# Performance work log

Hardware: AMD Instinct MI355X
Metric: run time of the kernel (lower is better)

The kernel has to match this reference:

```python
import jax, jax.numpy as jnp
import numpy as np

C = 256
G = 32  # GroupNorm groups
EPS = 1e-6


def setup_inputs() -> dict:
    key = jax.random.key(0)
    ks = jax.random.split(key, 11)
    B, H, W = 4, 64, 64
    scale = 0.02
    return {
        "x": jax.random.normal(ks[0], (B, C, H, W), dtype=jnp.float32),
        "gn_scale": jnp.ones((C,), jnp.float32),
        "gn_bias": jnp.zeros((C,), jnp.float32),
        "wq": jax.random.normal(ks[1], (C, C), jnp.float32) * scale,
        "bq": jnp.zeros((C,), jnp.float32),
        "wk": jax.random.normal(ks[2], (C, C), jnp.float32) * scale,
        "bk": jnp.zeros((C,), jnp.float32),
        "wv": jax.random.normal(ks[3], (C, C), jnp.float32) * scale,
        "bv": jnp.zeros((C,), jnp.float32),
        "wp": jax.random.normal(ks[4], (C, C), jnp.float32) * scale,
        "bp": jnp.zeros((C,), jnp.float32),
    }


def _group_norm(x, scale, bias):
    b, c, h, w = x.shape
    xr = x.reshape(b, G, c // G, h, w)
    mu = jnp.mean(xr, axis=(2, 3, 4), keepdims=True)
    var = jnp.var(xr, axis=(2, 3, 4), keepdims=True)
    xn = ((xr - mu) * jax.lax.rsqrt(var + EPS)).reshape(b, c, h, w)
    return xn * scale[None, :, None, None] + bias[None, :, None, None]


def _conv1x1(x, w, bch):
    # 1x1 conv == channel-mixing matmul; w is (out_ch, in_ch)
    return jnp.einsum('bchw,dc->bdhw', x, w) + bch[None, :, None, None]


def reference(x, gn_scale, gn_bias, wq, bq, wk, bk, wv, bv, wp, bp):
    b, c, h, w = x.shape
    hn = _group_norm(x, gn_scale, gn_bias)
    q = _conv1x1(hn, wq, bq).reshape(b, c, h * w)  # (b,c,N)
    k = _conv1x1(hn, wk, bk).reshape(b, c, h * w)
    v = _conv1x1(hn, wv, bv).reshape(b, c, h * w)
    # attn[b,i,j] = softmax_j( q_i . k_j / sqrt(c) )
    attn = jax.nn.softmax(jnp.einsum('bci,bcj->bij', q, k) * (c ** -0.5), axis=-1)
    A = jnp.einsum('bcj,bij->bci', v, attn).reshape(b, c, h, w)
    return x + _conv1x1(A, wp, bp)
```

## Files before the change

### kernel.cpp

```cpp
#include <hip/hip_runtime.h>
#include <stdint.h>

#define Bn 4
#define Cn 256
#define Gn 32
#define Nn 4096
#define CGn 8

typedef unsigned short u16;
typedef __attribute__((ext_vector_type(8))) short short8;
typedef __attribute__((ext_vector_type(4))) short short4v;
typedef __attribute__((ext_vector_type(4))) float f32x4;
typedef __attribute__((ext_vector_type(16))) float f32x16;

__device__ __forceinline__ u16 f2bf(float x) {
  uint32_t u = __float_as_uint(x);
  u += 0x7fffu + ((u >> 16) & 1u);
  return (u16)(u >> 16);
}
__device__ __forceinline__ float b2f(u16 v) {
  return __uint_as_float(((uint32_t)v) << 16);
}

__device__ __forceinline__ void gl_lds16(const void* g, void* l) {
  __builtin_amdgcn_global_load_lds(
      (__attribute__((address_space(1))) void*)(uintptr_t)g,
      (__attribute__((address_space(3))) void*)(uintptr_t)l, 16, 0, 0);
}

__device__ __forceinline__ int sw512(int row, int cb) { return row * 512 + ((cb ^ (row & 7)) * 16); }

__global__ void k_cs(const float* __restrict__ wq, const float* __restrict__ wk,
                     const float* __restrict__ wv, const float* __restrict__ wp,
                     const float* __restrict__ bq, const float* __restrict__ bk,
                     const float* __restrict__ bv, const float* __restrict__ x,
                     u16* __restrict__ wqkv, u16* __restrict__ wpb,
                     float* __restrict__ bqkv, float* __restrict__ stats) {
  if (blockIdx.x < 256) {
    const float s = 0.09016844005556021f;
    int i = blockIdx.x * 256 + threadIdx.x;
    wqkv[i]          = f2bf(wq[i] * s);
    wqkv[i + 65536]  = f2bf(wk[i]);
    wqkv[i + 131072] = f2bf(wv[i]);
    wpb[i]           = f2bf(wp[i]);
    if (i < 256) { bqkv[i] = bq[i] * s; bqkv[i + 256] = bk[i]; bqkv[i + 512] = bv[i]; }
  } else {
    int blk = blockIdx.x - 256;
    int grp = blk >> 2, part = blk & 3;
    const float4* base = (const float4*)(x + (size_t)grp * (CGn * Nn) + part * 8192);
    float s = 0.f, s2 = 0.f;
    for (int i = threadIdx.x; i < 2048; i += 256) {
      float4 v = base[i];
      s  += v.x + v.y + v.z + v.w;
      s2 += v.x * v.x + v.y * v.y + v.z * v.z + v.w * v.w;
    }
#pragma unroll
    for (int m = 1; m < 64; m <<= 1) { s += __shfl_xor(s, m, 64); s2 += __shfl_xor(s2, m, 64); }
    __shared__ float ps[4], ps2[4];
    int w = threadIdx.x >> 6;
    if ((threadIdx.x & 63) == 0) { ps[w] = s; ps2[w] = s2; }
    __syncthreads();
    if (threadIdx.x == 0) {
      stats[grp * 8 + part * 2]     = ps[0] + ps[1] + ps[2] + ps[3];
      stats[grp * 8 + part * 2 + 1] = ps2[0] + ps2[1] + ps2[2] + ps2[3];
    }
  }
}

__global__ void k_apply(const float* __restrict__ x, const float* __restrict__ stats,
                        const float* __restrict__ gsc, const float* __restrict__ gbi,
                        u16* __restrict__ hnT) {
  __shared__ __align__(16) char smem[32768];
  __shared__ float smu[Gn], srs[Gn];
  int n0 = blockIdx.x * 64;
  int b = blockIdx.y;
  int tid = threadIdx.x;
  if (tid < Gn) {
    float S = 0.f, S2 = 0.f;
#pragma unroll
    for (int p = 0; p < 4; ++p) {
      S  += stats[(b * Gn + tid) * 8 + p * 2];
      S2 += stats[(b * Gn + tid) * 8 + p * 2 + 1];
    }
    const float inv = 1.f / (CGn * Nn);
    float mu = S * inv;
    float var = S2 * inv - mu * mu;
    smu[tid] = mu;
    srs[tid] = rsqrtf(var + 1e-6f);
  }
  __syncthreads();
  int nl = (tid & 15) * 4;
  int cbase = tid >> 4;
  for (int pass = 0; pass < 16; ++pass) {
    int c = pass * 16 + cbase;
    float4 v = *(const float4*)(x + (size_t)b * Cn * Nn + (size_t)c * Nn + n0 + nl);
    int g = c >> 3;
    float sc = gsc[c] * srs[g];
    float bi = gbi[c] - smu[g] * sc;
    float vals[4] = {v.x, v.y, v.z, v.w};
#pragma unroll
    for (int i = 0; i < 4; ++i) {
      int row = nl + i;
      int off = row * 512 + ((((c >> 3) + row) & 31) * 16) + (c & 7) * 2;
      *(u16*)(smem + off) = f2bf(vals[i] * sc + bi);
    }
  }
  __syncthreads();
#pragma unroll
  for (int p = 0; p < 8; ++p) {
    int idx = p * 256 + tid;
    int row = idx >> 5, pc = idx & 31;
    int gc = (pc - row) & 31;
    short8 v8 = *(const short8*)(smem + row * 512 + pc * 16);
    *(short8*)(hnT + ((size_t)b * Nn + n0 + row) * Cn + gc * 8) = v8;
  }
}

__global__ __launch_bounds__(256, 2)
void k_qkv(const u16* __restrict__ wqkv, const float* __restrict__ bqkv,
           const u16* __restrict__ hnT, u16* __restrict__ qT, u16* __restrict__ kT,
           u16* __restrict__ vv) {
  __shared__ __align__(16) char smem[65536];
  const int tid = threadIdx.x, lane = tid & 63, w = tid >> 6;
  const int quad = (lane >> 4) & 3, low = lane & 15;
  const int d0 = blockIdx.y * 64, b = blockIdx.z;
  const int n_base = blockIdx.x * 256;
  const int which = d0 >> 8;
  const int dl0 = d0 & 255;
  const u16* hb = hnT + (size_t)b * Nn * Cn;
  const int scol = lane & 31;

#define QKV_STAGE(bsel, nt)                                                     \
  {                                                                             \
    _Pragma("unroll") for (int s = 0; s < 8; ++s) {                             \
      int r = w * 16 + s * 2 + (lane >> 5);                                     \
      int gc = (scol - r) & 31;                                                 \
      gl_lds16(hb + (size_t)(n_base + (nt) * 64 + r) * Cn + gc * 8,             \
               smem + (bsel) * 32768 + (w * 16 + s * 2) * 512);                 \
    }                                                                           \
  }

  QKV_STAGE(0, 0);
  short8 af[8];
  {
    const u16* wrow = wqkv + (size_t)(d0 + w * 16 + low) * Cn + quad * 8;
#pragma unroll
    for (int kk = 0; kk < 8; ++kk) af[kk] = *(const short8*)(wrow + kk * 32);
  }
  float bias[4];
#pragma unroll
  for (int r = 0; r < 4; ++r) bias[r] = bqkv[d0 + w * 16 + quad * 4 + r];

  for (int nt = 0; nt < 4; ++nt) {
    if (nt < 3) {
      QKV_STAGE((nt + 1) & 1, nt + 1);
      asm volatile("s_waitcnt vmcnt(10)" ::: "memory");
    } else {
      asm volatile("s_waitcnt vmcnt(0)" ::: "memory");
    }
    asm volatile("s_barrier" ::: "memory");
    char* buf = smem + (nt & 1) * 32768;
    f32x4 acc[4] = {{0.f,0.f,0.f,0.f},{0.f,0.f,0.f,0.f},{0.f,0.f,0.f,0.f},{0.f,0.f,0.f,0.f}};
#pragma unroll
    for (int kk = 0; kk < 8; ++kk)
#pragma unroll
      for (int t = 0; t < 4; ++t) {
        int row = t * 16 + low;
        short8 bf = *(const short8*)(buf + row * 512 + (((kk * 4 + quad) + row) & 31) * 16);
        acc[t] = __builtin_amdgcn_mfma_f32_16x16x32_bf16(af[kk], bf, acc[t], 0, 0, 0);
      }
    asm volatile("s_barrier" ::: "memory");
    char* Q = buf + w * 8192;
    if (which == 2) {
#pragma unroll
      for (int t = 0; t < 4; ++t)
#pragma unroll
        for (int rp = 0; rp < 2; ++rp) {
          uint32_t wv2;
          float f0 = acc[t][2 * rp] + bias[2 * rp];
          float f1 = acc[t][2 * rp + 1] + bias[2 * rp + 1];
          asm("v_cvt_pk_bf16_f32 %0, %1, %2" : "=v"(wv2) : "v"(f0), "v"(f1));
          *(u16*)(Q + (quad * 4 + 2 * rp) * 144 + t * 32 + low * 2) = (u16)wv2;
          *(u16*)(Q + (quad * 4 + 2 * rp + 1) * 144 + t * 32 + low * 2) = (u16)(wv2 >> 16);
        }
#pragma unroll
      for (int s = 0; s < 2; ++s) {
        int slot = s * 64 + lane;
        int row = slot >> 3, ch = slot & 7;
        short8 v8 = *(const short8*)(Q + row * 144 + ch * 16);
        *(short8*)(vv + (size_t)b * Cn * Nn + (size_t)(dl0 + w * 16 + row) * Nn +
                   n_base + nt * 64 + ch * 8) = v8;
      }
    } else {
#pragma unroll
      for (int t = 0; t < 4; ++t) {
        union { uint32_t u[2]; short4v s; } pk;
        float f0 = acc[t][0] + bias[0], f1 = acc[t][1] + bias[1];
        float f2 = acc[t][2] + bias[2], f3 = acc[t][3] + bias[3];
        asm("v_cvt_pk_bf16_f32 %0, %1, %2" : "=v"(pk.u[0]) : "v"(f0), "v"(f1));
        asm("v_cvt_pk_bf16_f32 %0, %1, %2" : "=v"(pk.u[1]) : "v"(f2), "v"(f3));
        *(short4v*)(Q + (t * 16 + low) * 48 + quad * 8) = pk.s;
      }
      u16* dst = (which == 0 ? qT : kT) + (size_t)b * Nn * Cn;
#pragma unroll
      for (int s = 0; s < 2; ++s) {
        int slot = s * 64 + lane;
        int row = slot >> 1, half = slot & 1;
        short8 v8 = *(const short8*)(Q + row * 48 + half * 16);
        *(short8*)(dst + (size_t)(n_base + nt * 64 + row) * Cn + dl0 + w * 16 + half * 8) = v8;
      }
    }
  }
#undef QKV_STAGE
}

__device__ __forceinline__ void flash_stage(char* smem, int bsel, const u16* kTb,
                                            const u16* vb, int j0, int w, int lo,
                                            int kr, int vr, int vp) {
  char* ksb = smem + bsel * 32768;
  char* vsb = ksb + 16384;
#pragma unroll
  for (int s = 0; s < 4; ++s) {
    int j = kr + s * 2;
    int gc = (lo - j) & 31;
    gl_lds16(kTb + (size_t)(j0 + j) * Cn + gc * 8, ksb + (w * 8 + s * 2) * 512);
  }
#pragma unroll
  for (int s = 0; s < 4; ++s) {
    int c = vr + s * 16;
    int gc = (vp - c - (c >> 2)) & 3;
    gl_lds16(vb + (size_t)c * Nn + j0 + gc * 8, vsb + (w * 64 + s * 16) * 64);
  }
}

__global__ __launch_bounds__(256, 2)
void k_flash(const u16* __restrict__ qT, const u16* __restrict__ kT,
             const u16* __restrict__ vv, u16* __restrict__ Op0,
             u16* __restrict__ Op1, u16* __restrict__ Op2, u16* __restrict__ Op3,
             float* __restrict__ lrow) {
  __shared__ __align__(16) char smem[65536];
  const int tid = threadIdx.x, lane = tid & 63, w = tid >> 6;
  const int lo = lane & 31, hi = lane >> 5;
  const int i0 = blockIdx.x * 128;
  const int b = blockIdx.y, jh = blockIdx.z;
  const u16* qTb = qT + (size_t)b * Nn * Cn;
  const u16* kTb = kT + (size_t)b * Nn * Cn;
  const u16* vb  = vv + (size_t)b * Cn * Nn;
  const int u7 = lo + hi;
  const int u9 = lo + hi + (lo >> 2);
  const int kr = w * 8 + hi;
  const int vr = w * 64 + (lane >> 2);
  const int vp = lane & 3;

  flash_stage(smem, 0, kTb, vb, jh * 1024, w, lo, kr, vr, vp);

  short8 qf[16];
  {
    const u16* qrow = qTb + (size_t)(i0 + w * 32 + lo) * Cn + hi * 8;
#pragma unroll
    for (int ks = 0; ks < 16; ++ks) qf[ks] = *(const short8*)(qrow + ks * 16);
  }
  f32x16 Oa[8];
#pragma unroll
  for (int ct = 0; ct < 8; ++ct)
#pragma unroll
    for (int e = 0; e < 16; ++e) Oa[ct][e] = 0.f;
  float l_ = 0.f;

  for (int jt = 0; jt < 32; ++jt) {
    if (jt < 31) {
      flash_stage(smem, (jt + 1) & 1, kTb, vb, jh * 1024 + (jt + 1) * 32, w, lo, kr, vr, vp);
      asm volatile("s_waitcnt vmcnt(8)" ::: "memory");
    } else {
      asm volatile("s_waitcnt vmcnt(0)" ::: "memory");
    }
    asm volatile("s_barrier" ::: "memory");
    const char* ksb = smem + (jt & 1) * 32768;
    const char* vsb = ksb + 16384;

    f32x16 S0;
#pragma unroll
    for (int e = 0; e < 16; ++e) S0[e] = 0.f;
    __builtin_amdgcn_s_setprio(1);
#pragma unroll
    for (int ks = 0; ks < 16; ++ks) {
      int ch = (ks * 2 + u7) & 31;
      short8 a0 = *(const short8*)(ksb + lo * 512 + ch * 16);
      S0 = __builtin_amdgcn_mfma_f32_32x32x16_bf16(a0, qf[ks], S0, 0, 0, 0);
    }
    __builtin_amdgcn_s_setprio(0);
    uint32_t Pp[8];
#pragma unroll
    for (int g = 0; g < 8; ++g) {
      float p0 = __builtin_amdgcn_exp2f(S0[2 * g]);
      float p1 = __builtin_amdgcn_exp2f(S0[2 * g + 1]);
      l_ += p0 + p1;
      asm("v_cvt_pk_bf16_f32 %0, %1, %2" : "=v"(Pp[g]) : "v"(p0), "v"(p1));
    }
#pragma unroll
    for (int kst = 0; kst < 2; ++kst) {
      uint32_t x0 = Pp[4 * kst], x1 = Pp[4 * kst + 1];
      uint32_t y0 = Pp[4 * kst + 2], y1 = Pp[4 * kst + 3];
      asm("v_permlane32_swap_b32 %0, %1" : "+v"(x0), "+v"(y0));
      asm("v_permlane32_swap_b32 %0, %1" : "+v"(x1), "+v"(y1));
      union { uint32_t u[4]; short8 s8; } pu;
      pu.u[0] = x0;
      pu.u[1] = x1;
      pu.u[2] = y0;
      pu.u[3] = y1;
      int ch = (kst * 2 + u9) & 3;
      __builtin_amdgcn_s_setprio(1);
#pragma unroll
      for (int ct = 0; ct < 8; ++ct) {
        short8 vf = *(const short8*)(vsb + (ct * 32 + lo) * 64 + ch * 16);
        Oa[ct] = __builtin_amdgcn_mfma_f32_32x32x16_bf16(vf, pu.s8, Oa[ct], 0, 0, 0);
      }
      __builtin_amdgcn_s_setprio(0);
    }
    asm volatile("s_barrier" ::: "memory");
  }

  l_ += __shfl_xor(l_, 32, 64);
  if (hi == 0)
    lrow[(size_t)jh * (Bn * Nn) + (size_t)b * Nn + i0 + w * 32 + lo] = l_;
  float invl = __builtin_amdgcn_rcpf(l_);
  __syncthreads();
#pragma unroll
  for (int ct = 0; ct < 8; ++ct)
#pragma unroll
    for (int g = 0; g < 4; ++g) {
      union { uint32_t u[2]; short4v s; } pk;
      float f0 = Oa[ct][g * 4 + 0] * invl, f1 = Oa[ct][g * 4 + 1] * invl;
      float f2 = Oa[ct][g * 4 + 2] * invl, f3 = Oa[ct][g * 4 + 3] * invl;
      asm("v_cvt_pk_bf16_f32 %0, %1, %2" : "=v"(pk.u[0]) : "v"(f0), "v"(f1));
      asm("v_cvt_pk_bf16_f32 %0, %1, %2" : "=v"(pk.u[1]) : "v"(f2), "v"(f3));
      int chv = (ct * 4 + g + lo) & 31;
      *(short4v*)(smem + w * 16384 + lo * 512 + chv * 16 + hi * 8) = pk.s;
    }
  __syncthreads();
  u16* Opj = (jh == 0) ? Op0 : (jh == 1) ? Op1 : (jh == 2) ? Op2 : Op3;
  u16* Ob = Opj + ((size_t)b * Nn + i0 + w * 32) * (size_t)Cn;
#pragma unroll
  for (int s = 0; s < 16; ++s) {
    int rr = s * 2 + hi;
    short8 v8 = *(const short8*)(smem + w * 16384 + rr * 512 + lo * 16);
    int gc = (lo - rr) & 31;
    *(short8*)(Ob + (size_t)rr * Cn + gc * 8) = v8;
  }
}

__global__ __launch_bounds__(256, 2)
void k_proj(const u16* __restrict__ wpb, const float* __restrict__ bp,
            const u16* __restrict__ O0, const u16* __restrict__ O1,
            const u16* __restrict__ O2, const u16* __restrict__ O3,
            const float* __restrict__ lrow,
            const float* __restrict__ x, float* __restrict__ out) {
  __shared__ __align__(16) char smem[65536];
  int tid = threadIdx.x, lane = tid & 63, w = tid >> 6, quad = lane >> 4, low = lane & 15;
  int n0 = blockIdx.x * 64, d0 = blockIdx.y * 64, b = blockIdx.z;
  {
    int r0 = w * 16;
#pragma unroll
    for (int s = 0; s < 8; ++s) {
      int rs = r0 + s * 2;
      int r = rs + (lane >> 5);
      int cb = (lane & 31) ^ (r & 7);
      gl_lds16(wpb + (size_t)(d0 + r) * Cn + cb * 8, smem + rs * 512);
    }
  }
#pragma unroll 4
  for (int p = 0; p < 8; ++p) {
    int slot = p * 256 + tid;
    int row = slot >> 5, pc = slot & 31;
    int gcb = pc ^ (row & 7);
    size_t gbase = ((size_t)b * Nn + n0 + row) * Cn + gcb * 8;
    short8 a0 = *(const short8*)(O0 + gbase);
    short8 a1 = *(const short8*)(O1 + gbase);
    short8 a2 = *(const short8*)(O2 + gbase);
    short8 a3 = *(const short8*)(O3 + gbase);
    int rrow = b * Nn + n0 + row;
    float L = lrow[rrow] + lrow[Bn * Nn + rrow] + lrow[2 * Bn * Nn + rrow] +
              lrow[3 * Bn * Nn + rrow];
    float inv = __builtin_amdgcn_rcpf(L);
    short8 o;
#pragma unroll
    for (int i = 0; i < 8; ++i)
      o[i] = (short)f2bf((b2f((u16)a0[i]) + b2f((u16)a1[i]) + b2f((u16)a2[i]) +
                          b2f((u16)a3[i])) * inv);
    *(short8*)(smem + 32768 + row * 512 + pc * 16) = o;
  }
  asm volatile("s_waitcnt vmcnt(0)" ::: "memory");
  __syncthreads();
  f32x4 acc[4] = {{0.f,0.f,0.f,0.f},{0.f,0.f,0.f,0.f},{0.f,0.f,0.f,0.f},{0.f,0.f,0.f,0.f}};
#pragma unroll
  for (int kk = 0; kk < 8; ++kk) {
    short8 af = *(const short8*)(smem + sw512(w * 16 + low, kk * 4 + quad));
#pragma unroll
    for (int t = 0; t < 4; ++t) {
      short8 bf = *(const short8*)(smem + 32768 + sw512(t * 16 + low, kk * 4 + quad));
      acc[t] = __builtin_amdgcn_mfma_f32_16x16x32_bf16(af, bf, acc[t], 0, 0, 0);
    }
  }
  int dloc = d0 + w * 16 + quad * 4;
#pragma unroll
  for (int t = 0; t < 4; ++t)
#pragma unroll
    for (int r = 0; r < 4; ++r) {
      size_t idx = (size_t)b * Cn * Nn + (size_t)(dloc + r) * Nn + n0 + t * 16 + low;
      out[idx] = x[idx] + acc[t][r] + bp[dloc + r];
    }
}

extern "C" void kernel_launch(void* const* d_in, const int* in_sizes, int n_in,
                              void* d_out, int out_size, void* d_ws, size_t ws_size,
                              hipStream_t stream) {
  const float* x   = (const float*)d_in[0];
  const float* gsc = (const float*)d_in[1];
  const float* gbi = (const float*)d_in[2];
  const float* wq  = (const float*)d_in[3];
  const float* bq  = (const float*)d_in[4];
  const float* wk  = (const float*)d_in[5];
  const float* bk  = (const float*)d_in[6];
  const float* wv  = (const float*)d_in[7];
  const float* bv  = (const float*)d_in[8];
  const float* wp  = (const float*)d_in[9];
  const float* bp  = (const float*)d_in[10];
  float* out = (float*)d_out;

  char* ws = (char*)d_ws;
  u16*   wqkv  = (u16*)(ws + 0);
  u16*   wpb   = (u16*)(ws + 393216);
  float* bqkv  = (float*)(ws + 524288);
  float* stats = (float*)(ws + 527360);
  float* lrow  = (float*)(ws + 532480);
  u16*   hnT   = (u16*)(ws + 1048576);
  u16*   qT    = (u16*)(ws + 9437184);
  u16*   kT    = (u16*)(ws + 17825792);
  u16*   vv    = (u16*)(ws + 26214400);
  u16*   Op1   = (u16*)(ws + 34603008);
  u16*   Op2   = (u16*)(ws + 42991616);
  u16*   Op3   = (u16*)(ws + 51380224);

  k_cs<<<768, 256, 0, stream>>>(wq, wk, wv, wp, bq, bk, bv, x, wqkv, wpb, bqkv, stats);
  k_apply<<<dim3(64, 4), 256, 0, stream>>>(x, stats, gsc, gbi, hnT);
  k_qkv<<<dim3(16, 12, 4), 256, 0, stream>>>(wqkv, bqkv, hnT, qT, kT, vv);
  k_flash<<<dim3(32, 4, 4), 256, 0, stream>>>(qT, kT, vv, hnT , Op1, Op2, Op3, lrow);
  k_proj<<<dim3(64, 4, 4), 256, 0, stream>>>(wpb, bp, hnT , Op1, Op2, Op3, lrow, x, out);
}
```

Baseline: 191.2 us.

## Fuse GroupNorm apply into QKV projection kernel, dropping hnT intermediate

Removes the separate k_apply kernel. k_qkv now reads fp32 x directly, normalizes it with the group stats, converts it to bf16 into LDS, and runs the MFMA projection on that tile, so the bf16 hnT buffer is never written or read back. The async double-buffered LDS staging is replaced by synchronous loads with barriers, shared memory shrinks, and launch bounds rise to 3 blocks per SM. The trade-off is redundant work: each of the 12 d-blocks re-reads and re-normalizes the same x tile, raising global fp32 traffic and losing load/compute overlap.

```diff
diff --git a/kernel.cpp b/kernel.cpp
--- a/kernel.cpp
+++ b/kernel.cpp
@@ -67,80 +67,35 @@
   }
 }
 
-__global__ void k_apply(const float* __restrict__ x, const float* __restrict__ stats,
-                        const float* __restrict__ gsc, const float* __restrict__ gbi,
-                        u16* __restrict__ hnT) {
-  __shared__ __align__(16) char smem[32768];
-  __shared__ float smu[Gn], srs[Gn];
-  int n0 = blockIdx.x * 64;
-  int b = blockIdx.y;
-  int tid = threadIdx.x;
-  if (tid < Gn) {
-    float S = 0.f, S2 = 0.f;
-#pragma unroll
-    for (int p = 0; p < 4; ++p) {
-      S  += stats[(b * Gn + tid) * 8 + p * 2];
-      S2 += stats[(b * Gn + tid) * 8 + p * 2 + 1];
-    }
-    const float inv = 1.f / (CGn * Nn);
-    float mu = S * inv;
-    float var = S2 * inv - mu * mu;
-    smu[tid] = mu;
-    srs[tid] = rsqrtf(var + 1e-6f);
-  }
-  __syncthreads();
-  int nl = (tid & 15) * 4;
-  int cbase = tid >> 4;
-  for (int pass = 0; pass < 16; ++pass) {
-    int c = pass * 16 + cbase;
-    float4 v = *(const float4*)(x + (size_t)b * Cn * Nn + (size_t)c * Nn + n0 + nl);
-    int g = c >> 3;
-    float sc = gsc[c] * srs[g];
-    float bi = gbi[c] - smu[g] * sc;
-    float vals[4] = {v.x, v.y, v.z, v.w};
-#pragma unroll
-    for (int i = 0; i < 4; ++i) {
-      int row = nl + i;
-      int off = row * 512 + ((((c >> 3) + row) & 31) * 16) + (c & 7) * 2;
-      *(u16*)(smem + off) = f2bf(vals[i] * sc + bi);
-    }
-  }
-  __syncthreads();
-#pragma unroll
-  for (int p = 0; p < 8; ++p) {
-    int idx = p * 256 + tid;
-    int row = idx >> 5, pc = idx & 31;
-    int gc = (pc - row) & 31;
-    short8 v8 = *(const short8*)(smem + row * 512 + pc * 16);
-    *(short8*)(hnT + ((size_t)b * Nn + n0 + row) * Cn + gc * 8) = v8;
-  }
-}
-
-__global__ __launch_bounds__(256, 2)
+__global__ __launch_bounds__(256, 3)
 void k_qkv(const u16* __restrict__ wqkv, const float* __restrict__ bqkv,
-           const u16* __restrict__ hnT, u16* __restrict__ qT, u16* __restrict__ kT,
-           u16* __restrict__ vv) {
-  __shared__ __align__(16) char smem[65536];
+           const float* __restrict__ x, const float* __restrict__ stats,
+           const float* __restrict__ gsc, const float* __restrict__ gbi,
+           u16* __restrict__ qT, u16* __restrict__ kT, u16* __restrict__ vv) {
+  __shared__ __align__(16) char smem[45312];
   const int tid = threadIdx.x, lane = tid & 63, w = tid >> 6;
   const int quad = (lane >> 4) & 3, low = lane & 15;
   const int d0 = blockIdx.y * 64, b = blockIdx.z;
   const int n_base = blockIdx.x * 256;
   const int which = d0 >> 8;
   const int dl0 = d0 & 255;
-  const u16* hb = hnT + (size_t)b * Nn * Cn;
-  const int scol = lane & 31;
-
-#define QKV_STAGE(bsel, nt)                                                     \
-  {                                                                             \
-    _Pragma("unroll") for (int s = 0; s < 8; ++s) {                             \
-      int r = w * 16 + s * 2 + (lane >> 5);                                     \
-      int gc = (scol - r) & 31;                                                 \
-      gl_lds16(hb + (size_t)(n_base + (nt) * 64 + r) * Cn + gc * 8,             \
-               smem + (bsel) * 32768 + (w * 16 + s * 2) * 512);                 \
-    }                                                                           \
-  }
-
-  QKV_STAGE(0, 0);
+  float* smu = (float*)(smem + 45056);
+  float* srs = (float*)(smem + 45184);
+
+  if (tid < Gn) {
+    float S = 0.f, S2 = 0.f;
+#pragma unroll
+    for (int p = 0; p < 4; ++p) {
+      S  += stats[(b * Gn + tid) * 8 + p * 2];
+      S2 += stats[(b * Gn + tid) * 8 + p * 2 + 1];
+    }
+    const float inv = 1.f / (CGn * Nn);
+    float mu = S * inv;
+    float var = S2 * inv - mu * mu;
+    smu[tid] = mu;
+    srs[tid] = rsqrtf(var + 1e-6f);
+  }
+
   short8 af[8];
   {
     const u16* wrow = wqkv + (size_t)(d0 + w * 16 + low) * Cn + quad * 8;
@@ -150,27 +105,40 @@
   float bias[4];
 #pragma unroll
   for (int r = 0; r < 4; ++r) bias[r] = bqkv[d0 + w * 16 + quad * 4 + r];
+  __syncthreads();
+
+  const int nl = (tid & 15) * 4;
+  const int cbase = tid >> 4;
+  char* Q = smem + 32768 + w * 3072;
 
   for (int nt = 0; nt < 4; ++nt) {
-    if (nt < 3) {
-      QKV_STAGE((nt + 1) & 1, nt + 1);
-      asm volatile("s_waitcnt vmcnt(10)" ::: "memory");
-    } else {
-      asm volatile("s_waitcnt vmcnt(0)" ::: "memory");
-    }
-    asm volatile("s_barrier" ::: "memory");
-    char* buf = smem + (nt & 1) * 32768;
+    if (nt) __syncthreads();
+    int nw = n_base + nt * 64;
+#pragma unroll
+    for (int pass = 0; pass < 16; ++pass) {
+      int c = pass * 16 + cbase;
+      float4 v = *(const float4*)(x + (size_t)b * Cn * Nn + (size_t)c * Nn + nw + nl);
+      int g = c >> 3;
+      float sc = gsc[c] * srs[g];
+      float bi = gbi[c] - smu[g] * sc;
+      float vals[4] = {v.x, v.y, v.z, v.w};
+#pragma unroll
+      for (int i = 0; i < 4; ++i) {
+        int row = nl + i;
+        int off = row * 512 + ((((c >> 3) + row) & 31) * 16) + (c & 7) * 2;
+        *(u16*)(smem + off) = f2bf(vals[i] * sc + bi);
+      }
+    }
+    __syncthreads();
     f32x4 acc[4] = {{0.f,0.f,0.f,0.f},{0.f,0.f,0.f,0.f},{0.f,0.f,0.f,0.f},{0.f,0.f,0.f,0.f}};
 #pragma unroll
     for (int kk = 0; kk < 8; ++kk)
 #pragma unroll
       for (int t = 0; t < 4; ++t) {
         int row = t * 16 + low;
-        short8 bf = *(const short8*)(buf + row * 512 + (((kk * 4 + quad) + row) & 31) * 16);
+        short8 bf = *(const short8*)(smem + row * 512 + (((kk * 4 + quad) + row) & 31) * 16);
         acc[t] = __builtin_amdgcn_mfma_f32_16x16x32_bf16(af[kk], bf, acc[t], 0, 0, 0);
       }
-    asm volatile("s_barrier" ::: "memory");
-    char* Q = buf + w * 8192;
     if (which == 2) {
 #pragma unroll
       for (int t = 0; t < 4; ++t)
@@ -211,7 +179,6 @@
       }
     }
   }
-#undef QKV_STAGE
 }
 
 __device__ __forceinline__ void flash_stage(char* smem, int bsel, const u16* kTb,
@@ -433,7 +400,7 @@
   float* bqkv  = (float*)(ws + 524288);
   float* stats = (float*)(ws + 527360);
   float* lrow  = (float*)(ws + 532480);
-  u16*   hnT   = (u16*)(ws + 1048576);
+  u16*   Op0   = (u16*)(ws + 1048576);
   u16*   qT    = (u16*)(ws + 9437184);
   u16*   kT    = (u16*)(ws + 17825792);
   u16*   vv    = (u16*)(ws + 26214400);
@@ -442,8 +409,7 @@
   u16*   Op3   = (u16*)(ws + 51380224);
 
   k_cs<<<768, 256, 0, stream>>>(wq, wk, wv, wp, bq, bk, bv, x, wqkv, wpb, bqkv, stats);
-  k_apply<<<dim3(64, 4), 256, 0, stream>>>(x, stats, gsc, gbi, hnT);
-  k_qkv<<<dim3(16, 12, 4), 256, 0, stream>>>(wqkv, bqkv, hnT, qT, kT, vv);
-  k_flash<<<dim3(32, 4, 4), 256, 0, stream>>>(qT, kT, vv, hnT , Op1, Op2, Op3, lrow);
-  k_proj<<<dim3(64, 4, 4), 256, 0, stream>>>(wpb, bp, hnT , Op1, Op2, Op3, lrow, x, out);
-}
+  k_qkv<<<dim3(16, 12, 4), 256, 0, stream>>>(wqkv, bqkv, x, stats, gsc, gbi, qT, kT, vv);
+  k_flash<<<dim3(32, 4, 4), 256, 0, stream>>>(qT, kT, vv, Op0, Op1, Op2, Op3, lrow);
+  k_proj<<<dim3(64, 4, 4), 256, 0, stream>>>(wpb, bp, Op0, Op1, Op2, Op3, lrow, x, out);
+}
```

After: 268.3 us. +40.3%, slower.
